# Performance work log

Measured on AMD Instinct MI355X. Metric: run time of the kernel, lower is better.

## Reference

```python
import jax, jax.numpy as jnp
import numpy as np

B, R, C = 32, 32, 32
NB, NC = 2, 20
CH = 6 + 2 * (R + C) + 2 * NC      # 174 label channels
CHP = NB * CH                      # 348 pred channels


def setup_inputs() -> dict:
    key = jax.random.key(0)
    pred = jax.random.uniform(key, (B, R, C, CHP), dtype=jnp.float32)
    rng = np.random.default_rng(0)
    label = rng.random((B, R, C, CH)).astype(np.float32)
    # object flag: exactly 1.0 where a center exists (the code tests == 1)
    label[..., 0] = (rng.random((B, R, C)) < 0.15).astype(np.float32)
    # one-hot corner row / col pointers
    rc = rng.integers(0, R, (B, R, C))
    cc = rng.integers(0, C, (B, R, C))
    label[..., 6:6 + R] = np.eye(R, dtype=np.float32)[rc]
    label[..., 6 + R:6 + R + C] = np.eye(C, dtype=np.float32)[cc]
    return {"pred": pred, "label": jnp.asarray(label), "num_box": NB, "num_class": NC}


def _take(a, idx):
    # gather one channel per cell; idx: [B,R,C] int
    return jnp.take_along_axis(a, idx[..., None], axis=-1)[..., 0]


def _convbox_match(pred, label, nb, nc):
    Bs, Rs, Cs, ch = label.shape
    chp = pred.shape[-1]
    base = 6 + 2 * (Rs + Cs)
    f32 = pred.dtype
    b_idx = jnp.arange(Bs)[:, None, None]
    rowm = jnp.broadcast_to(jnp.arange(Rs)[None, :, None], (Bs, Rs, Cs))
    colm = jnp.broadcast_to(jnp.arange(Cs)[None, None, :], (Bs, Rs, Cs))
    flag = (label[..., 0] == 1.0)
    rowc = jnp.argmax(label[..., 6:6 + Rs], axis=-1)            # first index of one-hot
    colc = jnp.argmax(label[..., 6 + Rs:6 + Rs + Cs], axis=-1)
    Lc = label[b_idx, rowc, colc]   # [B,R,C,ch]  values at corner cell
    Pc = pred[b_idx, rowc, colc]    # [B,R,C,chp]

    # ground-truth box per cell
    xm_t = (label[..., 2] + colm) / Cs
    ym_t = (label[..., 3] + rowm) / Rs
    xc_t = (Lc[..., 4] + colc) / Cs
    yc_t = (Lc[..., 5] + rowc) / Rs
    tw = jnp.abs(xm_t - xc_t) * 2.0
    th = jnp.abs(ym_t - yc_t) * 2.0

    scores = []
    for i in range(nb):
        sm = base * nb + i * nc
        sc = (base + nc) * nb + i * nc
        cat = (jnp.sum((pred[..., sm:sm + nc] - label[..., base:base + nc]) ** 2, -1)
               + jnp.sum((Pc[..., sc:sc + nc] - Lc[..., base + nc:base + 2 * nc]) ** 2, -1))
        conn_m = (_take(pred, 6 * nb + i * (Rs + Cs) + rowc)
                  * _take(pred, 6 * nb + i * (Rs + Cs) + Rs + colc))
        conn_c = (_take(Pc, (6 + Rs + Cs) * nb + i * (Rs + Cs) + rowm)
                  * _take(Pc, (6 + Rs + Cs) * nb + i * (Rs + Cs) + Rs + colm))
        conn = (conn_m + conn_c) / 2.0
        # faithful to source: channel index literally offset by colm / rowm
        xm_p = _take(pred, (nb + i) * 2 + 0 + colm) / Cs
        ym_p = _take(pred, (nb + i) * 2 + 1 + rowm) / Rs
        xc_p = _take(Pc, (nb * 2 + i) * 2 + 0 + colc) / Cs
        yc_p = _take(Pc, (nb * 2 + i) * 2 + 1 + rowc) / Rs
        ow = jnp.abs(xm_p - xc_p) * 2.0
        oh = jnp.abs(ym_p - yc_p) * 2.0
        w = jnp.minimum(xm_p + ow / 2, xm_t + tw / 2) - jnp.maximum(xm_p - ow / 2, xm_t - tw / 2)
        h = jnp.minimum(ym_p + oh / 2, ym_t + th / 2) - jnp.maximum(ym_p - oh / 2, ym_t - th / 2)
        inter = jnp.where((w < 0) | (h < 0), 0.0, w * h)
        union = ow * oh + tw * th - inter
        iou = inter / union
        rmse = (xm_p - xm_t) ** 2 + (ym_p - ym_t) ** 2 + (ow - tw) ** 2 + (oh - th) ** 2
        scores.append(conn * (iou - rmse + 0.1) + 0.1 * (2.0 - cat))
    best = jnp.argmax(jnp.stack(scores, axis=-1), axis=-1)  # [B,R,C] (first max, matches strict > update)

    val = flag.astype(f32)
    pred_mask = jnp.zeros((Bs, Rs, Cs, chp), f32)
    label_mask = jnp.zeros((Bs, Rs, Cs, ch), f32)
    ar_rc = jnp.arange(Rs + Cs)
    ar_nc = jnp.arange(nc)
    two = jnp.array([0, 1])
    bb = best[..., None]
    for n, (rt, ct) in enumerate([(rowm, colm), (rowc, colc)]):
        pch = jnp.concatenate([
            n * nb + bb,
            ((1 + n) * nb + bb) * 2 + two,
            (6 + n * (Rs + Cs)) * nb + bb * (Rs + Cs) + ar_rc,
            (base + n * nc) * nb + bb * nc + ar_nc,
        ], axis=-1)  # [B,R,C,3+R+C+nc]
        lch = jnp.concatenate([
            jnp.full((Bs, Rs, Cs, 1), n, dtype=jnp.int32),
            jnp.broadcast_to(2 * (1 + n) + two, (Bs, Rs, Cs, 2)),
            jnp.broadcast_to(6 + n * (Rs + Cs) + ar_rc, (Bs, Rs, Cs, Rs + Cs)),
            jnp.broadcast_to(base + n * nc + ar_nc, (Bs, Rs, Cs, nc)),
        ], axis=-1)
        # scatter 1s only at flagged cells; max() makes duplicates/overlaps a no-op
        pred_mask = pred_mask.at[b_idx[..., None], rt[..., None], ct[..., None], pch].max(val[..., None])
        label_mask = label_mask.at[b_idx[..., None], rt[..., None], ct[..., None], lch].max(val[..., None])
    return pred_mask, label_mask, label_mask


def reference(pred, label, num_box, num_class):
    return _convbox_match(pred, label, num_box, num_class)
```

## Files before the change

kernel.cpp:

```cpp
#include <hip/hip_runtime.h>

#define Bdim 32
#define Rdim 32
#define Cdim 32
#define NBOX 2
#define NCLS 20
#define CH   174
#define CHP  348
#define BASE 134

__global__ __launch_bounds__(256) void convbox_match_kernel(
    const float* __restrict__ pred, const float* __restrict__ label,
    float* __restrict__ out0,
    float* __restrict__ out1,
    float* __restrict__ out2)
{
    const int wave = (blockIdx.x << 2) | (threadIdx.x >> 6);
    const int lane = threadIdx.x & 63;
    const int c = wave & 31;
    const int r = (wave >> 5) & 31;
    const int b = wave >> 10;

    const float* Lcell = label + (size_t)wave * CH;

    if (Lcell[0] != 1.0f) return;

    float vr = (lane < 32) ? Lcell[6 + lane] : 0.0f;
    float vc = (lane < 32) ? Lcell[6 + 32 + lane] : 0.0f;
    unsigned long long mr = __ballot(lane < 32 && vr == 1.0f);
    unsigned long long mc = __ballot(lane < 32 && vc == 1.0f);
    const int rowc = mr ? (int)__builtin_ctzll(mr) : 0;
    const int colc = mc ? (int)__builtin_ctzll(mc) : 0;

    const int cornIdx = (b * Rdim + rowc) * Cdim + colc;
    const float* Lcorn = label + (size_t)cornIdx * CH;
    const float* Pcell = pred + (size_t)wave * CHP;
    const float* Pcorn = pred + (size_t)cornIdx * CHP;

    const float inv = 0.03125f;
    float xm_t = (Lcell[2] + (float)c) * inv;
    float ym_t = (Lcell[3] + (float)r) * inv;
    float xc_t = (Lcorn[4] + (float)colc) * inv;
    float yc_t = (Lcorn[5] + (float)rowc) * inv;
    float tw = fabsf(xm_t - xc_t) * 2.0f;
    float th = fabsf(ym_t - yc_t) * 2.0f;

    float score[NBOX];
#pragma unroll
    for (int i = 0; i < NBOX; ++i) {
        float cat = 0.0f;
#pragma unroll
        for (int k = 0; k < NCLS; ++k) {
            float d1 = Pcell[268 + i * NCLS + k] - Lcell[BASE + k];
            float d2 = Pcorn[308 + i * NCLS + k] - Lcorn[BASE + NCLS + k];
            cat += d1 * d1 + d2 * d2;
        }
        float conn_m = Pcell[12 + i * 64 + rowc] * Pcell[12 + i * 64 + 32 + colc];
        float conn_c = Pcorn[140 + i * 64 + r]   * Pcorn[140 + i * 64 + 32 + c];
        float conn = (conn_m + conn_c) * 0.5f;
        float xm_p = Pcell[(NBOX + i) * 2 + 0 + c] * inv;
        float ym_p = Pcell[(NBOX + i) * 2 + 1 + r] * inv;
        float xc_p = Pcorn[(NBOX * 2 + i) * 2 + 0 + colc] * inv;
        float yc_p = Pcorn[(NBOX * 2 + i) * 2 + 1 + rowc] * inv;
        float ow = fabsf(xm_p - xc_p) * 2.0f;
        float oh = fabsf(ym_p - yc_p) * 2.0f;
        float w = fminf(xm_p + ow * 0.5f, xm_t + tw * 0.5f)
                - fmaxf(xm_p - ow * 0.5f, xm_t - tw * 0.5f);
        float h = fminf(ym_p + oh * 0.5f, ym_t + th * 0.5f)
                - fmaxf(ym_p - oh * 0.5f, ym_t - th * 0.5f);
        float inter = (w < 0.0f || h < 0.0f) ? 0.0f : w * h;
        float uni = ow * oh + tw * th - inter;
        float iou = inter / uni;
        float rmse = (xm_p - xm_t) * (xm_p - xm_t) + (ym_p - ym_t) * (ym_p - ym_t)
                   + (ow - tw) * (ow - tw) + (oh - th) * (oh - th);
        score[i] = conn * (iou - rmse + 0.1f) + 0.1f * (2.0f - cat);
    }
    const int best = (score[1] > score[0]) ? 1 : 0;

#pragma unroll
    for (int n = 0; n < 2; ++n) {
        const int rt = n ? rowc : r;
        const int ct = n ? colc : c;
        const int tcell = (b * Rdim + rt) * Cdim + ct;

        float* pm = out0 + (size_t)tcell * CHP;
        if (lane == 0) pm[n * NBOX + best] = 1.0f;
        if (lane < 2)  pm[(1 + n) * NBOX * 2 + 2 * best + lane] = 1.0f;
        pm[(6 + n * 64) * NBOX + 64 * best + lane] = 1.0f;
        if (lane < NCLS) pm[(BASE + n * NCLS) * NBOX + NCLS * best + lane] = 1.0f;

        float* l1 = out1 + (size_t)tcell * CH;
        float* l2 = out2 + (size_t)tcell * CH;
        if (lane == 0) { l1[n] = 1.0f; l2[n] = 1.0f; }
        if (lane < 2)  { l1[2 * (1 + n) + lane] = 1.0f; l2[2 * (1 + n) + lane] = 1.0f; }
        l1[6 + n * 64 + lane] = 1.0f;
        l2[6 + n * 64 + lane] = 1.0f;
        if (lane < NCLS) { l1[BASE + n * NCLS + lane] = 1.0f; l2[BASE + n * NCLS + lane] = 1.0f; }
    }
}

extern "C" void kernel_launch(void* const* d_in, const int* in_sizes, int n_in,
                              void* d_out, int out_size, void* d_ws, size_t ws_size,
                              hipStream_t stream) {
    const float* pred  = (const float*)d_in[0];
    const float* label = (const float*)d_in[1];

    float* out0 = (float*)d_out;
    float* out1 = out0 + (size_t)Bdim * Rdim * Cdim * CHP;
    float* out2 = out1 + (size_t)Bdim * Rdim * Cdim * CH;

    hipMemsetAsync(d_out, 0, (size_t)out_size * sizeof(float), stream);

    const int n_cells = Bdim * Rdim * Cdim;
    const int blocks = n_cells / 4;
    convbox_match_kernel<<<blocks, 256, 0, stream>>>(pred, label, out0, out1, out2);
}
```

Measured before the change: 149.4 us.

## Replace memset and scattered stores with per-cell bitmask plus dense vectorized emit

The match kernel now records only a small per-cell bitmask in a global device array, set with atomicOr for the cell flag, the chosen box and the corner hits. A second kernel writes every output cell exactly once with float4/float2 stores, deriving ones and zeros from that mask. This removes the full-output memset and the scattered per-lane stores. It adds a second launch and a global scratch array, which the emit kernel resets so the next call starts clean.

```diff
diff --git a/kernel.cpp b/kernel.cpp
--- a/kernel.cpp
+++ b/kernel.cpp
@@ -8,12 +8,12 @@
 #define CH   174
 #define CHP  348
 #define BASE 134
+#define NCELL (Bdim * Rdim * Cdim)
 
-__global__ __launch_bounds__(256) void convbox_match_kernel(
-    const float* __restrict__ pred, const float* __restrict__ label,
-    float* __restrict__ out0,
-    float* __restrict__ out1,
-    float* __restrict__ out2)
+__device__ unsigned g_mask[NCELL];
+
+__global__ __launch_bounds__(256) void match_kernel(
+    const float* __restrict__ pred, const float* __restrict__ label)
 {
     const int wave = (blockIdx.x << 2) | (threadIdx.x >> 6);
     const int lane = threadIdx.x & 63;
@@ -77,25 +77,86 @@
     }
     const int best = (score[1] > score[0]) ? 1 : 0;
 
+    if (lane == 0) {
+        atomicOr(g_mask + wave,    1u | ((unsigned)best << 1));
+        atomicOr(g_mask + cornIdx, 4u << best);
+    }
+}
+
+__device__ __forceinline__ bool in_rng(int d, int lo, int n) {
+    return (unsigned)(d - lo) < (unsigned)n;
+}
+
+__global__ __launch_bounds__(256) void emit_kernel(
+    float* __restrict__ out0,
+    float* __restrict__ out1,
+    float* __restrict__ out2)
+{
+    const int cell = (blockIdx.x << 2) | (threadIdx.x >> 6);
+    const int lane = threadIdx.x & 63;
+
+    const unsigned m = g_mask[cell];
+    if (lane == 0) g_mask[cell] = 0;
+
+    float4* pm4 = (float4*)(out0 + (size_t)cell * CHP);
+    float2* l1  = (float2*)(out1 + (size_t)cell * CH);
+    float2* l2  = (float2*)(out2 + (size_t)cell * CH);
+
+    if (m == 0) {
+        const float4 z4 = make_float4(0.f, 0.f, 0.f, 0.f);
+        const float2 z2 = make_float2(0.f, 0.f);
 #pragma unroll
-    for (int n = 0; n < 2; ++n) {
-        const int rt = n ? rowc : r;
-        const int ct = n ? colc : c;
-        const int tcell = (b * Rdim + rt) * Cdim + ct;
+        for (int k = 0; k < 2; ++k) {
+            int i = lane + (k << 6);
+            if (i < 87) { pm4[i] = z4; l1[i] = z2; l2[i] = z2; }
+        }
+        return;
+    }
 
-        float* pm = out0 + (size_t)tcell * CHP;
-        if (lane == 0) pm[n * NBOX + best] = 1.0f;
-        if (lane < 2)  pm[(1 + n) * NBOX * 2 + 2 * best + lane] = 1.0f;
-        pm[(6 + n * 64) * NBOX + 64 * best + lane] = 1.0f;
-        if (lane < NCLS) pm[(BASE + n * NCLS) * NBOX + NCLS * best + lane] = 1.0f;
+    const int flag = m & 1;
+    const int b0   = (m >> 1) & 1;
+    const int c0   = (m >> 2) & 1;
+    const int c1   = (m >> 3) & 1;
+    const int cc   = c0 | c1;
 
-        float* l1 = out1 + (size_t)tcell * CH;
-        float* l2 = out2 + (size_t)tcell * CH;
-        if (lane == 0) { l1[n] = 1.0f; l2[n] = 1.0f; }
-        if (lane < 2)  { l1[2 * (1 + n) + lane] = 1.0f; l2[2 * (1 + n) + lane] = 1.0f; }
-        l1[6 + n * 64 + lane] = 1.0f;
-        l2[6 + n * 64 + lane] = 1.0f;
-        if (lane < NCLS) { l1[BASE + n * NCLS + lane] = 1.0f; l2[BASE + n * NCLS + lane] = 1.0f; }
+#pragma unroll
+    for (int k = 0; k < 2; ++k) {
+        int i = lane + (k << 6);
+        if (i < 87) {
+            float v[4];
+#pragma unroll
+            for (int j = 0; j < 4; ++j) {
+                int d = (i << 2) + j;
+                bool s = false;
+                if (flag) s = (d == b0) | in_rng(d, 4 + 2 * b0, 2)
+                            | in_rng(d, 12 + 64 * b0, 64) | in_rng(d, 268 + 20 * b0, 20);
+                if (c0)   s |= (d == 2) | in_rng(d, 8, 2)
+                            | in_rng(d, 140, 64) | in_rng(d, 308, 20);
+                if (c1)   s |= (d == 3) | in_rng(d, 10, 2)
+                            | in_rng(d, 204, 64) | in_rng(d, 328, 20);
+                v[j] = s ? 1.0f : 0.0f;
+            }
+            pm4[i] = make_float4(v[0], v[1], v[2], v[3]);
+        }
+    }
+
+#pragma unroll
+    for (int k = 0; k < 2; ++k) {
+        int i = lane + (k << 6);
+        if (i < 87) {
+            float v[2];
+#pragma unroll
+            for (int j = 0; j < 2; ++j) {
+                int d = (i << 1) + j;
+                bool s = false;
+                if (flag) s = (d == 0) | in_rng(d, 2, 2) | in_rng(d, 6, 64) | in_rng(d, 134, 20);
+                if (cc)   s |= (d == 1) | in_rng(d, 4, 2) | in_rng(d, 70, 64) | in_rng(d, 154, 20);
+                v[j] = s ? 1.0f : 0.0f;
+            }
+            float2 p = make_float2(v[0], v[1]);
+            l1[i] = p;
+            l2[i] = p;
+        }
     }
 }
 
@@ -109,9 +170,7 @@
     float* out1 = out0 + (size_t)Bdim * Rdim * Cdim * CHP;
     float* out2 = out1 + (size_t)Bdim * Rdim * Cdim * CH;
 
-    hipMemsetAsync(d_out, 0, (size_t)out_size * sizeof(float), stream);
-
-    const int n_cells = Bdim * Rdim * Cdim;
-    const int blocks = n_cells / 4;
-    convbox_match_kernel<<<blocks, 256, 0, stream>>>(pred, label, out0, out1, out2);
+    const int blocks = NCELL / 4;
+    match_kernel<<<blocks, 256, 0, stream>>>(pred, label);
+    emit_kernel<<<blocks, 256, 0, stream>>>(out0, out1, out2);
 }
```

Result: no change. 150.5 us (+0.7%).
